# Performance work log

Measured on AMD Instinct MI355X. Metric: run time of the kernel, lower is better.

Reference implementation:

```python
import jax, jax.numpy as jnp
import numpy as np

B, S, D = 2, 1024, 1024
N_HEADS = 16
R = 128
M = 8
N_NEURONS = 256


def group_gate(gate, n_basis):
    # gate: [B,S,N] -> [B,S,M], sum over consecutive groups, then normalize
    b, s, n = gate.shape
    gs = n // n_basis  # exact by construction (256/8)
    g = gate.reshape(b, s, n_basis, gs).sum(axis=-1)
    return g / (g.sum(axis=-1, keepdims=True) + 1e-8)


def feature_fn(x, neurons, weights):
    # x:[B,S,D], neurons:[M,D,R], weights:[B,S,M] -> h:[B,S,R]
    all_h = jnp.einsum('bsd,mdr->bsmr', x, neurons)
    return jnp.einsum('bsmr,bsm->bsr', all_h, weights)


def restore_fn(h, neurons, weights):
    # h:[B,S,R], neurons:[M,R,D], weights:[B,S,M] -> [B,S,D]
    pre = jnp.einsum('bsr,bsm->bsmr', h, weights)
    return jnp.einsum('bsmr,mrd->bsd', pre, neurons)


def setup_inputs() -> dict:
    key = jax.random.key(0)
    ks = jax.random.split(key, 9)
    sc = 0.02
    return {
        'x': jax.random.normal(ks[0], (B, S, D), jnp.float32),
        'qk_f': jax.random.normal(ks[1], (M, D, R), jnp.float32) * sc,
        'qk_r': jax.random.normal(ks[2], (M, R, D), jnp.float32) * sc,
        'v_f': jax.random.normal(ks[3], (M, D, R), jnp.float32) * sc,
        'v_r': jax.random.normal(ks[4], (M, R, D), jnp.float32) * sc,
        'Wg_q': jax.random.normal(ks[5], (D, N_NEURONS), jnp.float32) * sc,
        'Wg_k': jax.random.normal(ks[6], (D, N_NEURONS), jnp.float32) * sc,
        'Wg_v': jax.random.normal(ks[7], (D, N_NEURONS), jnp.float32) * sc,
        'W_O': jax.random.normal(ks[8], (D, D), jnp.float32) * sc,
    }


def reference(x, qk_f, qk_r, v_f, v_r, Wg_q, Wg_k, Wg_v, W_O):
    # Router gates (softmax over neuron dim), then grouped per basis
    g_Q = jax.nn.softmax(jnp.einsum('bsd,dn->bsn', x, Wg_q), axis=-1)
    g_K = jax.nn.softmax(jnp.einsum('bsd,dn->bsn', x, Wg_k), axis=-1)
    g_V = jax.nn.softmax(jnp.einsum('bsd,dn->bsn', x, Wg_v), axis=-1)
    gQ_b = group_gate(g_Q, M)
    gK_b = group_gate(g_K, M)
    gV_b = group_gate(g_V, M)

    Q = restore_fn(feature_fn(x, qk_f, gQ_b), qk_r, gQ_b)
    K = restore_fn(feature_fn(x, qk_f, gK_b), qk_r, gK_b)
    V = restore_fn(feature_fn(x, v_f, gV_b), v_r, gV_b)

    d_head = D // N_HEADS
    Q = Q.reshape(B, S, N_HEADS, d_head).transpose(0, 2, 1, 3)
    K = K.reshape(B, S, N_HEADS, d_head).transpose(0, 2, 1, 3)
    V = V.reshape(B, S, N_HEADS, d_head).transpose(0, 2, 1, 3)

    scale = jnp.sqrt(jnp.float32(d_head))
    scores = jnp.einsum('bhsd,bhtd->bhst', Q, K) / scale
    causal = jnp.tril(jnp.ones((S, S), dtype=jnp.bool_))
    scores = jnp.where(causal, scores, jnp.finfo(scores.dtype).min)
    attn_w = jax.nn.softmax(scores, axis=-1)
    out = jnp.einsum('bhst,bhtd->bhsd', attn_w, V)
    out = out.transpose(0, 2, 1, 3).reshape(B, S, D)
    out = jnp.einsum('bsd,de->bse', out, W_O)
    return out
```

## Files before the change

kernel.cpp:

```cpp
#include <hip/hip_runtime.h>
#include <hip/hip_bf16.h>

#define BB 2
#define SS 1024
#define DD 1024
#define NH 16
#define DH 64
#define MM 8
#define RR 128
#define NN 256
#define NT (BB*SS)

using bf16 = __hip_bfloat16;

typedef __attribute__((ext_vector_type(8))) short short8;
typedef __attribute__((ext_vector_type(4))) short short4v;
typedef __attribute__((ext_vector_type(4))) float f32x4;

__device__ __forceinline__ void stf(float* p, size_t i, float v) { p[i] = v; }
__device__ __forceinline__ void stf(bf16* p, size_t i, float v) { p[i] = __float2bfloat16(v); }

#define GLD16(g, l) __builtin_amdgcn_global_load_lds( \
    (const __attribute__((address_space(1))) void*)(g), \
    (__attribute__((address_space(3))) void*)(l), 16, 0, 0)

__device__ __forceinline__ short8 lds_load8(const short* p) {
    short4v a = *(const short4v*)p;
    short4v b = *(const short4v*)(p + 4);
    short8 r;
    r[0] = a[0]; r[1] = a[1]; r[2] = a[2]; r[3] = a[3];
    r[4] = b[0]; r[5] = b[1]; r[6] = b[2]; r[7] = b[3];
    return r;
}

template <typename TC>
__device__ __forceinline__ void gemm64_body(
    const bf16* __restrict__ A, const bf16* __restrict__ Bt, TC* __restrict__ C,
    int Kdim, int Nz, int m0, int n0, bf16* As, bf16* Bs) {
    const int tid = threadIdx.x;
    const int wave = tid >> 6, lane = tid & 63;
    const int quad = lane >> 4, l15 = lane & 15;
    const int wr = wave >> 1, wc = wave & 1;

    f32x4 acc[2][4];
#pragma unroll
    for (int i = 0; i < 2; ++i)
#pragma unroll
        for (int j = 0; j < 4; ++j) acc[i][j] = (f32x4)0.f;

    for (int k0 = 0; k0 < Kdim; k0 += 64) {
        __syncthreads();
#pragma unroll
        for (int i = 0; i < 2; ++i) {
            const int L = i * 256 + wave * 64 + lane;
            const int row = L >> 3;
            const int gch = (L & 7) ^ ((row >> 1) & 7);
            GLD16(A + (size_t)(m0 + row) * Kdim + k0 + gch * 8, &As[(i * 256 + wave * 64) * 8]);
        }
#pragma unroll
        for (int i = 0; i < 4; ++i) {
            const int L = i * 256 + wave * 64 + lane;
            const int row = L >> 3;
            const int gch = (L & 7) ^ ((row >> 1) & 7);
            GLD16(Bt + (size_t)(n0 + row) * Kdim + k0 + gch * 8, &Bs[(i * 256 + wave * 64) * 8]);
        }
        __syncthreads();

#pragma unroll
        for (int kk = 0; kk < 2; ++kk) {
            short8 aF[2], bF[4];
#pragma unroll
            for (int bi = 0; bi < 2; ++bi) {
                int m = wr * 32 + bi * 16 + l15;
                int slot = (kk * 4 + quad) ^ ((m >> 1) & 7);
                aF[bi] = *(const short8*)&As[(m * 8 + slot) * 8];
            }
#pragma unroll
            for (int bj = 0; bj < 4; ++bj) {
                int n = wc * 64 + bj * 16 + l15;
                int slot = (kk * 4 + quad) ^ ((n >> 1) & 7);
                bF[bj] = *(const short8*)&Bs[(n * 8 + slot) * 8];
            }
#pragma unroll
            for (int bi = 0; bi < 2; ++bi)
#pragma unroll
                for (int bj = 0; bj < 4; ++bj)
                    acc[bi][bj] = __builtin_amdgcn_mfma_f32_16x16x32_bf16(aF[bi], bF[bj], acc[bi][bj], 0, 0, 0);
        }
    }

#pragma unroll
    for (int bi = 0; bi < 2; ++bi)
#pragma unroll
        for (int bj = 0; bj < 4; ++bj)
#pragma unroll
            for (int r = 0; r < 4; ++r) {
                int row = m0 + wr * 32 + bi * 16 + quad * 4 + r;
                int col = n0 + wc * 64 + bj * 16 + l15;
                stf(C, (size_t)row * Nz + col, acc[bi][bj][r]);
            }
}

struct GemmZ {
    const bf16* A[5];
    const bf16* Bt[5];
    void* C[5];
    int N[5];
};

__global__ __launch_bounds__(256) void mfma_proj(GemmZ P, int Kdim) {
    __shared__ bf16 As[64 * 64];
    __shared__ bf16 Bs[128 * 64];
    const int bidx = blockIdx.x;
    int z, xx, yy;
    if (bidx < 512) { z = bidx >> 8; int r = bidx & 255; yy = r >> 3; xx = r & 7; }
    else { int r = bidx - 512; z = 2 + r / 64; r = r % 64; yy = r >> 1; xx = r & 1; }
    gemm64_body<bf16>(P.A[z], P.Bt[z], (bf16*)P.C[z], Kdim, P.N[z], yy * 64, xx * 128, As, Bs);
}

__global__ __launch_bounds__(256) void mfma_restore(GemmZ P, int Kdim) {
    __shared__ bf16 As[64 * 64];
    __shared__ bf16 Bs[128 * 64];
    const int z = blockIdx.z;
    gemm64_body<bf16>(P.A[z], P.Bt[z], (bf16*)P.C[z], Kdim, P.N[z],
                      blockIdx.y * 64, blockIdx.x * 128, As, Bs);
}

__global__ __launch_bounds__(256) void mfma_gemm_64(
    const bf16* __restrict__ A, const bf16* __restrict__ Bt, float* __restrict__ C,
    int Kdim, int Ndim) {
    __shared__ bf16 As[64 * 64];
    __shared__ bf16 Bs[128 * 64];
    gemm64_body<float>(A, Bt, C, Kdim, Ndim, blockIdx.y * 64, blockIdx.x * 128, As, Bs);
}

struct ConvJobs {
    const float* src[9];
    bf16* dst[9];
    int K[9], R[9], G[9];
    int tEnd[9];
};

__global__ void convert_kernel(ConvJobs J) {
    __shared__ float tile[32][33];
    const int b = blockIdx.x;
    int j = 0;
    while (j < 8 && b >= J.tEnd[j]) ++j;
    const int local = b - (j > 0 ? J.tEnd[j - 1] : 0);
    const float* src = J.src[j];
    bf16* dst = J.dst[j];
    const int tid = threadIdx.x;

    if (J.G[j] == 0) {
        size_t base = (size_t)local * 4096 + (size_t)tid * 16;
        const float4* s4 = (const float4*)(src + base);
        short* d = (short*)(dst + base);
#pragma unroll
        for (int c = 0; c < 4; ++c) {
            float4 v = s4[c];
            short4v o;
            bf16 t0 = __float2bfloat16(v.x); o[0] = *(short*)&t0;
            bf16 t1 = __float2bfloat16(v.y); o[1] = *(short*)&t1;
            bf16 t2 = __float2bfloat16(v.z); o[2] = *(short*)&t2;
            bf16 t3 = __float2bfloat16(v.w); o[3] = *(short*)&t3;
            *(short4v*)(d + c * 4) = o;
        }
    } else {
        const int Kj = J.K[j], Rj = J.R[j];
        const int Rb = Rj >> 5, Kb = Kj >> 5;
        const int perG = Kb * Rb;
        const int g = local / perG;
        const int rem = local - g * perG;
        const int kb = rem / Rb, rb = rem - kb * Rb;
        const int tx = tid & 31, ty0 = tid >> 5;
        const float* s = src + ((size_t)(g * Kj + kb * 32) * Rj) + rb * 32 + tx;
#pragma unroll
        for (int p = 0; p < 4; ++p)
            tile[ty0 + p * 8][tx] = s[(size_t)(ty0 + p * 8) * Rj];
        __syncthreads();
        bf16* dd = dst + ((size_t)(g * Rj + rb * 32) * Kj) + kb * 32 + tx;
#pragma unroll
        for (int p = 0; p < 4; ++p)
            dd[(size_t)(ty0 + p * 8) * Kj] = __float2bfloat16(tile[tx][ty0 + p * 8]);
    }
}

__global__ void gate_combine(const bf16* __restrict__ logitsAll,
                             const bf16* __restrict__ allh,
                             bf16* __restrict__ preQ, bf16* __restrict__ preK,
                             bf16* __restrict__ preV) {
    const int t = blockIdx.x;
    const int n = threadIdx.x;
    const int wave = n >> 6, lane = n & 63;
    __shared__ float wred[3][4];
    __shared__ float sred[3][4];
    __shared__ float gred[3][8];

    float v[3], e[3];
#pragma unroll
    for (int z = 0; z < 3; ++z)
        v[z] = __bfloat162float(logitsAll[(size_t)z * NT * NN + (size_t)t * NN + n]);

    float mz[3];
#pragma unroll
    for (int z = 0; z < 3; ++z) {
        mz[z] = v[z];
#pragma unroll
        for (int off = 1; off <= 32; off <<= 1)
            mz[z] = fmaxf(mz[z], __shfl_xor(mz[z], off));
    }
    if (lane == 0) {
#pragma unroll
        for (int z = 0; z < 3; ++z) wred[z][wave] = mz[z];
    }
    __syncthreads();
    float gmax[3];
#pragma unroll
    for (int z = 0; z < 3; ++z)
        gmax[z] = fmaxf(fmaxf(wred[z][0], wred[z][1]), fmaxf(wred[z][2], wred[z][3]));

    float ws[3];
#pragma unroll
    for (int z = 0; z < 3; ++z) {
        e[z] = __expf(v[z] - gmax[z]);
        ws[z] = e[z];
#pragma unroll
        for (int off = 1; off <= 32; off <<= 1)
            ws[z] += __shfl_xor(ws[z], off);
    }
    if (lane == 0) {
#pragma unroll
        for (int z = 0; z < 3; ++z) sred[z][wave] = ws[z];
    }
    float gs[3];
#pragma unroll
    for (int z = 0; z < 3; ++z) {
        gs[z] = e[z];
#pragma unroll
        for (int off = 1; off <= 16; off <<= 1)
            gs[z] += __shfl_xor(gs[z], off);
    }
    __syncthreads();
    float total[3];
#pragma unroll
    for (int z = 0; z < 3; ++z)
        total[z] = sred[z][0] + sred[z][1] + sred[z][2] + sred[z][3];
    if ((n & 31) == 0) {
#pragma unroll
        for (int z = 0; z < 3; ++z) gred[z][n >> 5] = gs[z] / total[z];
    }
    __syncthreads();

    float gv[3][8];
#pragma unroll
    for (int z = 0; z < 3; ++z) {
        float tot = 0.f;
#pragma unroll
        for (int m = 0; m < 8; ++m) tot += gred[z][m];
        float inv = 1.0f / (tot + 1e-8f);
#pragma unroll
        for (int m = 0; m < 8; ++m) gv[z][m] = gred[z][m] * inv;
    }

    const int r0 = n & 127;
    const int half = n >> 7;
    const bf16* src_qk = allh + (size_t)t * 1024;
    const bf16* src_v  = allh + (size_t)NT * DD + (size_t)t * 1024;
    float hq = 0.f, hk = 0.f, hv = 0.f;
#pragma unroll
    for (int m = 0; m < 8; ++m) {
        float aqk = __bfloat162float(src_qk[m * 128 + r0]);
        float av  = __bfloat162float(src_v[m * 128 + r0]);
        hq += aqk * gv[0][m];
        hk += aqk * gv[1][m];
        hv += av  * gv[2][m];
    }
    __syncthreads();
#pragma unroll
    for (int mm = 0; mm < 4; ++mm) {
        int m = half * 4 + mm;
        size_t o = (size_t)t * 1024 + m * 128 + r0;
        preQ[o] = __float2bfloat16(hq * gv[0][m]);
        preK[o] = __float2bfloat16(hk * gv[1][m]);
        preV[o] = __float2bfloat16(hv * gv[2][m]);
    }
}

#define LDK 68

__global__ __launch_bounds__(256) void flash_attn_split(
    const bf16* __restrict__ Q, const bf16* __restrict__ K,
    const bf16* __restrict__ V, float* __restrict__ Opart,
    float* __restrict__ ml) {
    const int bx = blockIdx.x;
    const int c = bx & 511;
    const int second = bx >> 9;
    const int qt = second ? (c >> 5) : (15 - (c >> 5));
    const int half = second;
    const int bh = c & 31;
    const int b = bh >> 4;
    const int h = bh & 15;
    const int h0 = (qt + 2) >> 1;
    const int kt_lo = half ? h0 : 0;
    const int kt_hi = half ? (qt + 1) : h0;

    const int tid = threadIdx.x;
    const int wave = tid >> 6;
    const int lane = tid & 63;
    const int quad = lane >> 4;
    const int l15 = lane & 15;

    __shared__ short Ks[2][64 * 64];
    __shared__ short Vt[2][64 * LDK];
    __shared__ short Ps[4 * 16 * LDK];

    const int q_row = qt * 64 + wave * 16 + l15;
    const bf16* qptr = Q + (size_t)(b * SS + q_row) * DD + h * DH + quad * 8;
    short8 aq0 = *(const short8*)qptr;
    short8 aq1 = *(const short8*)(qptr + 32);

    const int krp = tid & 31;
    const int dhb = (tid >> 5) * 8;

    float m_r[4], l_r[4];
    f32x4 o[4];
#pragma unroll
    for (int r = 0; r < 4; ++r) { m_r[r] = -3.0e38f; l_r[r] = 0.f; }
#pragma unroll
    for (int cc = 0; cc < 4; ++cc) o[cc] = (f32x4)0.f;

    const float scale = 0.125f;

    if (kt_lo < kt_hi) {
#pragma unroll
        for (int i = 0; i < 2; ++i) {
            const int L = i * 256 + wave * 64 + lane;
            const int row = L >> 3;
            const int gch = (L & 7) ^ ((row >> 1) & 7);
            GLD16(K + (size_t)(b * SS + kt_lo * 64 + row) * DD + h * DH + gch * 8,
                  &Ks[0][(i * 256 + wave * 64) * 8]);
        }
        const bf16* s0 = V + (size_t)(b * SS + kt_lo * 64 + 2 * krp) * DD + h * DH + dhb;
        short8 r0 = *(const short8*)s0;
        short8 r1 = *(const short8*)(s0 + DD);
#pragma unroll
        for (int i = 0; i < 8; ++i) {
            unsigned int pk = (unsigned short)r0[i] | ((unsigned int)(unsigned short)r1[i] << 16);
            *(unsigned int*)&Vt[0][(dhb + i) * LDK + 2 * krp] = pk;
        }
        __syncthreads();
    }

    for (int kt = kt_lo; kt < kt_hi; ++kt) {
        const int buf = (kt - kt_lo) & 1;
        const bool pf = (kt + 1 < kt_hi);
        short8 pr0, pr1;
        if (pf) {
#pragma unroll
            for (int i = 0; i < 2; ++i) {
                const int L = i * 256 + wave * 64 + lane;
                const int row = L >> 3;
                const int gch = (L & 7) ^ ((row >> 1) & 7);
                GLD16(K + (size_t)(b * SS + (kt + 1) * 64 + row) * DD + h * DH + gch * 8,
                      &Ks[buf ^ 1][(i * 256 + wave * 64) * 8]);
            }
            const bf16* s0 = V + (size_t)(b * SS + (kt + 1) * 64 + 2 * krp) * DD + h * DH + dhb;
            pr0 = *(const short8*)s0;
            pr1 = *(const short8*)(s0 + DD);
        }

        const short* KsB = Ks[buf];
        f32x4 s[4];
#pragma unroll
        for (int cc = 0; cc < 4; ++cc) {
            int n = cc * 16 + l15;
            int sl0 = quad ^ ((n >> 1) & 7);
            int sl1 = (quad + 4) ^ ((n >> 1) & 7);
            short8 bk0 = *(const short8*)&KsB[(n * 8 + sl0) * 8];
            short8 bk1 = *(const short8*)&KsB[(n * 8 + sl1) * 8];
            f32x4 acc = (f32x4)0.f;
            acc = __builtin_amdgcn_mfma_f32_16x16x32_bf16(aq0, bk0, acc, 0, 0, 0);
            acc = __builtin_amdgcn_mfma_f32_16x16x32_bf16(aq1, bk1, acc, 0, 0, 0);
            s[cc] = acc;
        }

        const bool diag = (kt == qt);
#pragma unroll
        for (int cc = 0; cc < 4; ++cc) {
#pragma unroll
            for (int r = 0; r < 4; ++r) {
                float v = s[cc][r] * scale;
                if (diag) {
                    int row_rel = wave * 16 + quad * 4 + r;
                    int col_rel = cc * 16 + l15;
                    if (col_rel > row_rel) v = -3.0e38f;
                }
                s[cc][r] = v;
            }
        }

        float p[4][4];
        float alpha[4];
#pragma unroll
        for (int r = 0; r < 4; ++r) {
            float mx = fmaxf(fmaxf(s[0][r], s[1][r]), fmaxf(s[2][r], s[3][r]));
            mx = fmaxf(mx, __shfl_xor(mx, 1));
            mx = fmaxf(mx, __shfl_xor(mx, 2));
            mx = fmaxf(mx, __shfl_xor(mx, 4));
            mx = fmaxf(mx, __shfl_xor(mx, 8));
            float new_m = fmaxf(m_r[r], mx);
            alpha[r] = __expf(m_r[r] - new_m);
            float rs = 0.f;
#pragma unroll
            for (int cc = 0; cc < 4; ++cc) {
                float e = __expf(s[cc][r] - new_m);
                p[cc][r] = e;
                rs += e;
            }
            rs += __shfl_xor(rs, 1);
            rs += __shfl_xor(rs, 2);
            rs += __shfl_xor(rs, 4);
            rs += __shfl_xor(rs, 8);
            l_r[r] = l_r[r] * alpha[r] + rs;
            m_r[r] = new_m;
        }
#pragma unroll
        for (int cc = 0; cc < 4; ++cc)
#pragma unroll
            for (int r = 0; r < 4; ++r) o[cc][r] *= alpha[r];

        short* pw = &Ps[wave * 16 * LDK];
#pragma unroll
        for (int cc = 0; cc < 4; ++cc)
#pragma unroll
            for (int r = 0; r < 4; ++r) {
                bf16 hb = __float2bfloat16(p[cc][r]);
                pw[(quad * 4 + r) * LDK + cc * 16 + l15] = *(short*)&hb;
            }

        short8 ap0 = lds_load8(&pw[l15 * LDK + quad * 8]);
        short8 ap1 = lds_load8(&pw[l15 * LDK + 32 + quad * 8]);

        const short* VtB = Vt[buf];
#pragma unroll
        for (int cc = 0; cc < 4; ++cc) {
            short8 bv0 = lds_load8(&VtB[(cc * 16 + l15) * LDK + quad * 8]);
            short8 bv1 = lds_load8(&VtB[(cc * 16 + l15) * LDK + 32 + quad * 8]);
            o[cc] = __builtin_amdgcn_mfma_f32_16x16x32_bf16(ap0, bv0, o[cc], 0, 0, 0);
            o[cc] = __builtin_amdgcn_mfma_f32_16x16x32_bf16(ap1, bv1, o[cc], 0, 0, 0);
        }

        if (pf) {
#pragma unroll
            for (int i = 0; i < 8; ++i) {
                unsigned int pk = (unsigned short)pr0[i] | ((unsigned int)(unsigned short)pr1[i] << 16);
                *(unsigned int*)&Vt[buf ^ 1][(dhb + i) * LDK + 2 * krp] = pk;
            }
        }
        __syncthreads();
    }

    const int idx = (half * 32 + bh) * 16 + qt;
    float* ob = Opart + (size_t)idx * 4096;
#pragma unroll
    for (int cc = 0; cc < 4; ++cc)
#pragma unroll
        for (int r = 0; r < 4; ++r) {
            int row = wave * 16 + quad * 4 + r;
            ob[row * 64 + cc * 16 + l15] = o[cc][r];
        }
    if (l15 == 0) {
#pragma unroll
        for (int r = 0; r < 4; ++r) {
            int row = wave * 16 + quad * 4 + r;
            ml[(size_t)idx * 128 + row] = m_r[r];
            ml[(size_t)idx * 128 + 64 + row] = l_r[r];
        }
    }
}

__global__ void attn_combine(const float* __restrict__ Opart,
                             const float* __restrict__ ml,
                             bf16* __restrict__ out) {
    const int bidx = blockIdx.x;
    const int bh = bidx >> 4;
    const int qt = bidx & 15;
    const int b = bh >> 4;
    const int h = bh & 15;
    const int tid = threadIdx.x;
    const int row = tid >> 2;
    const int cg = tid & 3;

    const int p0 = bh * 16 + qt;
    const int p1 = 512 + bh * 16 + qt;
    float m0 = ml[(size_t)p0 * 128 + row], l0 = ml[(size_t)p0 * 128 + 64 + row];
    float m1 = ml[(size_t)p1 * 128 + row], l1 = ml[(size_t)p1 * 128 + 64 + row];
    float ms = fmaxf(m0, m1);
    float w0 = __expf(m0 - ms), w1 = __expf(m1 - ms);
    float inv = 1.0f / (l0 * w0 + l1 * w1);

    const float* o0 = Opart + (size_t)p0 * 4096 + row * 64 + cg * 16;
    const float* o1 = Opart + (size_t)p1 * 4096 + row * 64 + cg * 16;
    short out16[16];
#pragma unroll
    for (int j = 0; j < 16; j += 4) {
        float4 a = *(const float4*)(o0 + j);
        float4 bb = *(const float4*)(o1 + j);
        float v0 = (a.x * w0 + bb.x * w1) * inv;
        float v1 = (a.y * w0 + bb.y * w1) * inv;
        float v2 = (a.z * w0 + bb.z * w1) * inv;
        float v3 = (a.w * w0 + bb.w * w1) * inv;
        bf16 t0 = __float2bfloat16(v0); out16[j] = *(short*)&t0;
        bf16 t1 = __float2bfloat16(v1); out16[j + 1] = *(short*)&t1;
        bf16 t2 = __float2bfloat16(v2); out16[j + 2] = *(short*)&t2;
        bf16 t3 = __float2bfloat16(v3); out16[j + 3] = *(short*)&t3;
    }
    short* dst = (short*)(out + (size_t)(b * SS + qt * 64 + row) * DD + h * DH + cg * 16);
    *(short8*)dst = *(short8*)&out16[0];
    *(short8*)(dst + 8) = *(short8*)&out16[8];
}

extern "C" void kernel_launch(void* const* d_in, const int* in_sizes, int n_in,
                              void* d_out, int out_size, void* d_ws, size_t ws_size,
                              hipStream_t stream) {
    const float* x    = (const float*)d_in[0];
    const float* qk_f = (const float*)d_in[1];
    const float* qk_r = (const float*)d_in[2];
    const float* v_f  = (const float*)d_in[3];
    const float* v_r  = (const float*)d_in[4];
    const float* Wg_q = (const float*)d_in[5];
    const float* Wg_k = (const float*)d_in[6];
    const float* Wg_v = (const float*)d_in[7];
    const float* W_O  = (const float*)d_in[8];

    char* w = (char*)d_ws;
    const size_t MB = 1 << 20;
    bf16* xb     = (bf16*)(w + 0);
    bf16* wg_bt  = (bf16*)(w + 4 * MB);
    bf16* fbt    = (bf16*)(w + (size_t)(5.5 * MB));
    bf16* logits = (bf16*)(w + (size_t)(9.5 * MB));
    bf16* qkr_bt = (bf16*)(w + 16 * MB);
    bf16* vr_bt  = (bf16*)(w + 18 * MB);
    bf16* wo_bt  = (bf16*)(w + 20 * MB);
    bf16* preQ   = (bf16*)(w + 0);
    bf16* preK   = (bf16*)(w + 4 * MB);
    bf16* Kb     = (bf16*)(w + 8 * MB);
    bf16* Vb     = (bf16*)(w + 12 * MB);
    bf16* attnb  = (bf16*)(w + 0);
    float* Opart = (float*)(w + 32 * MB);
    float* mlbuf = (float*)(w + 48 * MB);
    bf16* allh   = (bf16*)d_out;
    bf16* preV   = allh + (size_t)NT * DD;
    bf16* Qb     = (bf16*)d_out;
    float* out   = (float*)d_out;

    ConvJobs J;
    J.src[0] = qk_f; J.dst[0] = fbt;              J.K[0] = 1024; J.R[0] = 128;  J.G[0] = 8;
    J.src[1] = v_f;  J.dst[1] = fbt + 1024*1024;  J.K[1] = 1024; J.R[1] = 128;  J.G[1] = 8;
    J.src[2] = qk_r; J.dst[2] = qkr_bt;           J.K[2] = 1024; J.R[2] = 1024; J.G[2] = 1;
    J.src[3] = v_r;  J.dst[3] = vr_bt;            J.K[3] = 1024; J.R[3] = 1024; J.G[3] = 1;
    J.src[4] = W_O;  J.dst[4] = wo_bt;            J.K[4] = 1024; J.R[4] = 1024; J.G[4] = 1;
    J.src[5] = Wg_q; J.dst[5] = wg_bt;            J.K[5] = 1024; J.R[5] = 256;  J.G[5] = 1;
    J.src[6] = Wg_k; J.dst[6] = wg_bt + 256*1024; J.K[6] = 1024; J.R[6] = 256;  J.G[6] = 1;
    J.src[7] = Wg_v; J.dst[7] = wg_bt + 2*256*1024; J.K[7] = 1024; J.R[7] = 256; J.G[7] = 1;
    J.src[8] = x;    J.dst[8] = xb;               J.K[8] = 0;    J.R[8] = 0;    J.G[8] = 0;
    int tiles[9] = {1024, 1024, 1024, 1024, 1024, 256, 256, 256, 512};
    int cum = 0;
    for (int i = 0; i < 9; ++i) { cum += tiles[i]; J.tEnd[i] = cum; }
    convert_kernel<<<cum, 256, 0, stream>>>(J);

    GemmZ Pp;
    Pp.A[0] = Pp.A[1] = Pp.A[2] = Pp.A[3] = Pp.A[4] = xb;
    Pp.Bt[0] = fbt;             Pp.Bt[1] = fbt + 1024*1024;
    Pp.Bt[2] = wg_bt;           Pp.Bt[3] = wg_bt + 256*1024;  Pp.Bt[4] = wg_bt + 2*256*1024;
    Pp.C[0] = allh;             Pp.C[1] = allh + (size_t)NT * DD;
    Pp.C[2] = logits;           Pp.C[3] = logits + (size_t)NT * NN;
    Pp.C[4] = logits + 2 * (size_t)NT * NN;
    Pp.N[0] = 1024; Pp.N[1] = 1024; Pp.N[2] = 256; Pp.N[3] = 256; Pp.N[4] = 256;
    mfma_proj<<<dim3(704), 256, 0, stream>>>(Pp, DD);

    gate_combine<<<NT, 256, 0, stream>>>(logits, allh, preQ, preK, preV);

    GemmZ Pr;
    Pr.A[0] = preQ; Pr.A[1] = preK; Pr.A[2] = preV;
    Pr.Bt[0] = qkr_bt; Pr.Bt[1] = qkr_bt; Pr.Bt[2] = vr_bt;
    Pr.C[0] = Qb; Pr.C[1] = Kb; Pr.C[2] = Vb;
    Pr.N[0] = Pr.N[1] = Pr.N[2] = 1024;
    Pr.A[3] = Pr.A[4] = nullptr; Pr.Bt[3] = Pr.Bt[4] = nullptr;
    Pr.C[3] = Pr.C[4] = nullptr; Pr.N[3] = Pr.N[4] = 0;
    mfma_restore<<<dim3(8, 32, 3), 256, 0, stream>>>(Pr, DD);

    flash_attn_split<<<dim3(1024), 256, 0, stream>>>(Qb, Kb, Vb, Opart, mlbuf);

    attn_combine<<<dim3(512), 256, 0, stream>>>(Opart, mlbuf, attnb);

    mfma_gemm_64<<<dim3(8, 32), 256, 0, stream>>>(attnb, wo_bt, out, DD, DD);
}
```

Before: 199.8 us.

## Replace split-KV flash attention plus combine with single-pass causal kernel

Removes the two-way KV split and the separate combine kernel. Each block now processes the whole causal key range for its query tile and normalizes and writes the bf16 output directly. This drops the fp32 partial-output round trip and one kernel launch. The cost is fewer blocks (512 instead of 1024) and a longer per-block critical path for late query tiles, which are scheduled first to balance load.

```diff
diff --git a/kernel.cpp b/kernel.cpp
--- a/kernel.cpp
+++ b/kernel.cpp
@@ -288,21 +288,15 @@
 
 #define LDK 68
 
-__global__ __launch_bounds__(256) void flash_attn_split(
+__global__ __launch_bounds__(256) void flash_attn_causal(
     const bf16* __restrict__ Q, const bf16* __restrict__ K,
-    const bf16* __restrict__ V, float* __restrict__ Opart,
-    float* __restrict__ ml) {
+    const bf16* __restrict__ V, bf16* __restrict__ out) {
     const int bx = blockIdx.x;
-    const int c = bx & 511;
-    const int second = bx >> 9;
-    const int qt = second ? (c >> 5) : (15 - (c >> 5));
-    const int half = second;
-    const int bh = c & 31;
+    const int qt = 15 - (bx >> 5);
+    const int bh = bx & 31;
     const int b = bh >> 4;
     const int h = bh & 15;
-    const int h0 = (qt + 2) >> 1;
-    const int kt_lo = half ? h0 : 0;
-    const int kt_hi = half ? (qt + 1) : h0;
+    const int kt_hi = qt + 1;
 
     const int tid = threadIdx.x;
     const int wave = tid >> 6;
@@ -331,16 +325,16 @@
 
     const float scale = 0.125f;
 
-    if (kt_lo < kt_hi) {
+    {
 #pragma unroll
         for (int i = 0; i < 2; ++i) {
             const int L = i * 256 + wave * 64 + lane;
             const int row = L >> 3;
             const int gch = (L & 7) ^ ((row >> 1) & 7);
-            GLD16(K + (size_t)(b * SS + kt_lo * 64 + row) * DD + h * DH + gch * 8,
+            GLD16(K + (size_t)(b * SS + row) * DD + h * DH + gch * 8,
                   &Ks[0][(i * 256 + wave * 64) * 8]);
         }
-        const bf16* s0 = V + (size_t)(b * SS + kt_lo * 64 + 2 * krp) * DD + h * DH + dhb;
+        const bf16* s0 = V + (size_t)(b * SS + 2 * krp) * DD + h * DH + dhb;
         short8 r0 = *(const short8*)s0;
         short8 r1 = *(const short8*)(s0 + DD);
 #pragma unroll
@@ -351,8 +345,8 @@
         __syncthreads();
     }
 
-    for (int kt = kt_lo; kt < kt_hi; ++kt) {
-        const int buf = (kt - kt_lo) & 1;
+    for (int kt = 0; kt < kt_hi; ++kt) {
+        const int buf = kt & 1;
         const bool pf = (kt + 1 < kt_hi);
         short8 pr0, pr1;
         if (pf) {
@@ -460,64 +454,17 @@
         __syncthreads();
     }
 
-    const int idx = (half * 32 + bh) * 16 + qt;
-    float* ob = Opart + (size_t)idx * 4096;
+    float inv[4];
+#pragma unroll
+    for (int r = 0; r < 4; ++r) inv[r] = 1.0f / l_r[r];
 #pragma unroll
     for (int cc = 0; cc < 4; ++cc)
 #pragma unroll
         for (int r = 0; r < 4; ++r) {
-            int row = wave * 16 + quad * 4 + r;
-            ob[row * 64 + cc * 16 + l15] = o[cc][r];
-        }
-    if (l15 == 0) {
-#pragma unroll
-        for (int r = 0; r < 4; ++r) {
-            int row = wave * 16 + quad * 4 + r;
-            ml[(size_t)idx * 128 + row] = m_r[r];
-            ml[(size_t)idx * 128 + 64 + row] = l_r[r];
-        }
-    }
-}
-
-__global__ void attn_combine(const float* __restrict__ Opart,
-                             const float* __restrict__ ml,
-                             bf16* __restrict__ out) {
-    const int bidx = blockIdx.x;
-    const int bh = bidx >> 4;
-    const int qt = bidx & 15;
-    const int b = bh >> 4;
-    const int h = bh & 15;
-    const int tid = threadIdx.x;
-    const int row = tid >> 2;
-    const int cg = tid & 3;
-
-    const int p0 = bh * 16 + qt;
-    const int p1 = 512 + bh * 16 + qt;
-    float m0 = ml[(size_t)p0 * 128 + row], l0 = ml[(size_t)p0 * 128 + 64 + row];
-    float m1 = ml[(size_t)p1 * 128 + row], l1 = ml[(size_t)p1 * 128 + 64 + row];
-    float ms = fmaxf(m0, m1);
-    float w0 = __expf(m0 - ms), w1 = __expf(m1 - ms);
-    float inv = 1.0f / (l0 * w0 + l1 * w1);
-
-    const float* o0 = Opart + (size_t)p0 * 4096 + row * 64 + cg * 16;
-    const float* o1 = Opart + (size_t)p1 * 4096 + row * 64 + cg * 16;
-    short out16[16];
-#pragma unroll
-    for (int j = 0; j < 16; j += 4) {
-        float4 a = *(const float4*)(o0 + j);
-        float4 bb = *(const float4*)(o1 + j);
-        float v0 = (a.x * w0 + bb.x * w1) * inv;
-        float v1 = (a.y * w0 + bb.y * w1) * inv;
-        float v2 = (a.z * w0 + bb.z * w1) * inv;
-        float v3 = (a.w * w0 + bb.w * w1) * inv;
-        bf16 t0 = __float2bfloat16(v0); out16[j] = *(short*)&t0;
-        bf16 t1 = __float2bfloat16(v1); out16[j + 1] = *(short*)&t1;
-        bf16 t2 = __float2bfloat16(v2); out16[j + 2] = *(short*)&t2;
-        bf16 t3 = __float2bfloat16(v3); out16[j + 3] = *(short*)&t3;
-    }
-    short* dst = (short*)(out + (size_t)(b * SS + qt * 64 + row) * DD + h * DH + cg * 16);
-    *(short8*)dst = *(short8*)&out16[0];
-    *(short8*)(dst + 8) = *(short8*)&out16[8];
+            int row = qt * 64 + wave * 16 + quad * 4 + r;
+            out[(size_t)(b * SS + row) * DD + h * DH + cc * 16 + l15] =
+                __float2bfloat16(o[cc][r] * inv[r]);
+        }
 }
 
 extern "C" void kernel_launch(void* const* d_in, const int* in_sizes, int n_in,
@@ -547,8 +494,6 @@
     bf16* Kb     = (bf16*)(w + 8 * MB);
     bf16* Vb     = (bf16*)(w + 12 * MB);
     bf16* attnb  = (bf16*)(w + 0);
-    float* Opart = (float*)(w + 32 * MB);
-    float* mlbuf = (float*)(w + 48 * MB);
     bf16* allh   = (bf16*)d_out;
     bf16* preV   = allh + (size_t)NT * DD;
     bf16* Qb     = (bf16*)d_out;
@@ -590,9 +535,7 @@
     Pr.C[3] = Pr.C[4] = nullptr; Pr.N[3] = Pr.N[4] = 0;
     mfma_restore<<<dim3(8, 32, 3), 256, 0, stream>>>(Pr, DD);
 
-    flash_attn_split<<<dim3(1024), 256, 0, stream>>>(Qb, Kb, Vb, Opart, mlbuf);
-
-    attn_combine<<<dim3(512), 256, 0, stream>>>(Opart, mlbuf, attnb);
+    flash_attn_causal<<<dim3(512), 256, 0, stream>>>(Qb, Kb, Vb, attnb);
 
     mfma_gemm_64<<<dim3(8, 32), 256, 0, stream>>>(attnb, wo_bt, out, DD, DD);
 }
```

After: 195.2 us. 2.3% less time.
